# Kernel tuning notes

Hardware: AMD Instinct MI355X
Metric: run time of the kernel (lower is better)

Reference implementation:

```python
import jax, jax.numpy as jnp
import numpy as np

NEG_SLOPE = 0.2  # PyG GATConv default negative_slope
N_NODES = 40000
N_EDGES = 640000
IN_DIM = 128
SAT_DIM = 64
HID = 128
OUT_DIM = 54


def gat_conv(x, edge_index, W, a_src, a_dst, bias):
    """PyG GATConv with heads=1, concat=True, add_self_loops=True."""
    n = x.shape[0]
    loops = jnp.arange(n, dtype=edge_index.dtype)
    src = jnp.concatenate([edge_index[0], loops])  # message sources j
    dst = jnp.concatenate([edge_index[1], loops])  # message targets i
    h = x @ W.T                                    # [N, C]
    alpha_s = h @ a_src                            # [N]
    alpha_d = h @ a_dst                            # [N]
    e = jax.nn.leaky_relu(alpha_s[src] + alpha_d[dst], NEG_SLOPE)  # [E]
    # segment softmax over incoming edges of each dst node (self-loops guarantee non-empty segments)
    m = jax.ops.segment_max(e, dst, num_segments=n)
    e = jnp.exp(e - m[dst])
    denom = jax.ops.segment_sum(e, dst, num_segments=n)
    alpha = e / (denom[dst] + 1e-16)
    out = jax.ops.segment_sum(alpha[:, None] * h[src], dst, num_segments=n)
    return out + bias


def setup_inputs() -> dict:
    key = jax.random.key(0)
    ks = jax.random.split(key, 16)
    s = lambda d: 1.0 / np.sqrt(d)
    inp = {
        "x": jax.random.normal(ks[0], (N_NODES, IN_DIM), jnp.float32),
        "edge_index": jax.random.randint(ks[1], (2, N_EDGES), 0, N_NODES, jnp.int32),
        "sat_W": jax.random.normal(ks[2], (HID, SAT_DIM), jnp.float32) * s(SAT_DIM),
        "sat_b": jnp.zeros((HID,), jnp.float32),
        "neigh_W": jax.random.normal(ks[3], (HID, IN_DIM - SAT_DIM), jnp.float32) * s(IN_DIM - SAT_DIM),
        "neigh_b": jnp.zeros((HID,), jnp.float32),
        "conv1_W": jax.random.normal(ks[4], (HID, HID), jnp.float32) * s(HID),
        "conv1_asrc": jax.random.normal(ks[5], (HID,), jnp.float32) * s(HID),
        "conv1_adst": jax.random.normal(ks[6], (HID,), jnp.float32) * s(HID),
        "conv1_b": jnp.zeros((HID,), jnp.float32),
        "conv2_W": jax.random.normal(ks[7], (HID, HID), jnp.float32) * s(HID),
        "conv2_asrc": jax.random.normal(ks[8], (HID,), jnp.float32) * s(HID),
        "conv2_adst": jax.random.normal(ks[9], (HID,), jnp.float32) * s(HID),
        "conv2_b": jnp.zeros((HID,), jnp.float32),
        "fc1_W": jax.random.normal(ks[10], (HID, HID), jnp.float32) * s(HID),
        "fc1_b": jnp.zeros((HID,), jnp.float32),
        "fc2_W": jax.random.normal(ks[11], (OUT_DIM, HID), jnp.float32) * s(HID),
        "fc2_b": jnp.zeros((OUT_DIM,), jnp.float32),
    }
    return inp


def reference(x, edge_index, sat_W, sat_b, neigh_W, neigh_b,
              conv1_W, conv1_asrc, conv1_adst, conv1_b,
              conv2_W, conv2_asrc, conv2_adst, conv2_b,
              fc1_W, fc1_b, fc2_W, fc2_b):
    sat = jax.nn.relu(x[:, :SAT_DIM] @ sat_W.T + sat_b)
    nei = jax.nn.relu(x[:, SAT_DIM:] @ neigh_W.T + neigh_b)
    h = sat + 0.5 * nei
    h = jax.nn.relu(gat_conv(h, edge_index, conv1_W, conv1_asrc, conv1_adst, conv1_b))
    h = jax.nn.relu(gat_conv(h, edge_index, conv2_W, conv2_asrc, conv2_adst, conv2_b))
    h = jax.nn.relu(h @ fc1_W.T + fc1_b)
    return h @ fc2_W.T + fc2_b
```

## Files before the change

kernel.cpp:

```cpp
#include <hip/hip_runtime.h>


#define N_NODES 40000
#define N_EDGES 640000
#define DIM     128

typedef unsigned short u16;
typedef __attribute__((ext_vector_type(8))) short bf16x8;
typedef __attribute__((ext_vector_type(4))) float f32x4;

__device__ __forceinline__ u16 f2bf(float v) {
    unsigned u = __float_as_uint(v);
    u += 0x7FFFu + ((u >> 16) & 1u);
    return (u16)(u >> 16);
}
__device__ __forceinline__ float bf2f(u16 h) { return __uint_as_float(((unsigned)h) << 16); }
__device__ __forceinline__ float rdlane_f(float v, int l) {
    return __uint_as_float(__builtin_amdgcn_readlane(__float_as_uint(v), l));
}

__device__ __forceinline__ int hswz(int row, int col) {
    return row * 128 + ((((col >> 2) ^ (row & 7))) << 2) + (col & 3);
}
__device__ __forceinline__ float4 hread4(const float* hbuf, int row, int k) {
    int b = (k >> 2) ^ (row & 7);
    return *(const float4*)&hbuf[row * 128 + (b << 2)];
}
__device__ __forceinline__ void split8(const float* vv, bf16x8& hi, bf16x8& lo) {
#pragma unroll
    for (int i = 0; i < 8; ++i) {
        u16 h = f2bf(vv[i]);
        hi[i] = (short)h;
        lo[i] = (short)f2bf(vv[i] - bf2f(h));
    }
}

__global__ __launch_bounds__(256) void k_wcvt(
    const float* __restrict__ satW, const float* __restrict__ neiW,
    const float* __restrict__ c1W, const float* __restrict__ c2W,
    const float* __restrict__ f1W, const float* __restrict__ f2W,
    u16* __restrict__ wa, int* __restrict__ deg, int* __restrict__ counter) {
    int gid = (blockIdx.y * gridDim.x + blockIdx.x) * 256 + threadIdx.x;
    if (gid < N_NODES) deg[gid] = 1;
    if (gid == 0) *counter = 0;

    int m = blockIdx.y;
    const float* src; int C, K, Cp; int offH, offL;
    switch (m) {
        case 0: src = satW; C = 128; K = 64;  Cp = 128; offH = 0;      offL = 8192;   break;
        case 1: src = neiW; C = 128; K = 64;  Cp = 128; offH = 16384;  offL = 24576;  break;
        case 2: src = c1W;  C = 128; K = 128; Cp = 128; offH = 32768;  offL = 49152;  break;
        case 3: src = c2W;  C = 128; K = 128; Cp = 128; offH = 65536;  offL = 81920;  break;
        case 4: src = f1W;  C = 128; K = 128; Cp = 128; offH = 98304;  offL = 114688; break;
        default:src = f2W;  C = 54;  K = 128; Cp = 64;  offH = 131072; offL = 139264; break;
    }
    int e = blockIdx.x * 256 + threadIdx.x;
    if (e >= Cp * K) return;
    int c = e / K, k = e - c * K;
    float v = (c < C) ? src[c * K + k] : 0.f;
    u16 h = f2bf(v);
    wa[offH + e] = h;
    wa[offL + e] = f2bf(v - bf2f(h));
}

__global__ void k_deg_count(const int* __restrict__ dst, int* __restrict__ deg) {
    int t = blockIdx.x * 256 + threadIdx.x;
    if (t < N_EDGES) atomicAdd(&deg[dst[t]], 1);
}
__global__ void k_assign(const int* __restrict__ deg, int* __restrict__ counter,
                         int* __restrict__ start, int* __restrict__ cursor,
                         int* __restrict__ csr_src) {
    int i = blockIdx.x * 256 + threadIdx.x;
    if (i >= N_NODES) return;
    int d = deg[i];
    int s = atomicAdd(counter, d);
    start[i] = s;
    csr_src[s] = i;
    cursor[i] = s + 1;
}
__global__ void k_fill_edges(const int* __restrict__ src, const int* __restrict__ dst,
                             int* __restrict__ cursor, int* __restrict__ csr_src) {
    int t = blockIdx.x * 256 + threadIdx.x;
    if (t < N_EDGES) {
        int p = atomicAdd(&cursor[dst[t]], 1);
        csr_src[p] = src[t];
    }
}

template<int CT>
__device__ __forceinline__ void stage_W(u16* Ws, const u16* __restrict__ Wh,
                                        const u16* __restrict__ Wl, int kc, int tid) {
    for (int idx = tid; idx < CT * 2 * 2 * 64; idx += 256) {
        int l = idx & 63;
        int q = idx >> 6;
        int hilo = q & 1;
        int ks = (q >> 1) & 1;
        int ct = q >> 2;
        int c = ct * 16 + (l & 15);
        int k = kc * 64 + ks * 32 + (l >> 4) * 8;
        const u16* Wp = hilo ? Wl : Wh;
        *reinterpret_cast<bf16x8*>(&Ws[idx * 8]) =
            *reinterpret_cast<const bf16x8*>(Wp + (size_t)c * 128 + k);
    }
}

#define MFMA3(ACC, AH, AL, BH, BL)                                             \
    ACC = __builtin_amdgcn_mfma_f32_16x16x32_bf16(AH, BH, ACC, 0, 0, 0);       \
    ACC = __builtin_amdgcn_mfma_f32_16x16x32_bf16(AH, BL, ACC, 0, 0, 0);       \
    ACC = __builtin_amdgcn_mfma_f32_16x16x32_bf16(AL, BH, ACC, 0, 0, 0);

__device__ __forceinline__ void alpha_epi(const f32x4* acc, int lane, int r0,
                                          const float* __restrict__ a_src,
                                          const float* __restrict__ a_dst,
                                          float* __restrict__ as_, float* __restrict__ ad_) {
    float ps[4] = {0, 0, 0, 0}, pd[4] = {0, 0, 0, 0};
#pragma unroll
    for (int ct = 0; ct < 8; ++ct) {
        float asv = a_src[ct * 16 + (lane & 15)];
        float adv = a_dst[ct * 16 + (lane & 15)];
#pragma unroll
        for (int r = 0; r < 4; ++r) {
            ps[r] = fmaf(acc[ct][r], asv, ps[r]);
            pd[r] = fmaf(acc[ct][r], adv, pd[r]);
        }
    }
#pragma unroll
    for (int off = 1; off < 16; off <<= 1) {
#pragma unroll
        for (int r = 0; r < 4; ++r) {
            ps[r] += __shfl_xor(ps[r], off);
            pd[r] += __shfl_xor(pd[r], off);
        }
    }
    if ((lane & 15) == 0) {
#pragma unroll
        for (int r = 0; r < 4; ++r) {
            int row = r0 + (lane >> 4) * 4 + r;
            as_[row] = ps[r];
            ad_[row] = pd[r];
        }
    }
}

__global__ __launch_bounds__(256) void k_enc_conv1(
    const float* __restrict__ x,
    const u16* __restrict__ sH, const u16* __restrict__ sL,
    const u16* __restrict__ nH, const u16* __restrict__ nL,
    const float* __restrict__ satb, const float* __restrict__ neib,
    const u16* __restrict__ Wh, const u16* __restrict__ Wl,
    const float* __restrict__ a_src, const float* __restrict__ a_dst,
    u16* __restrict__ outG, float* __restrict__ as_, float* __restrict__ ad_)
{
    __shared__ u16 Wbuf[16384];
    __shared__ float hbuf[8192];
    const int tid = threadIdx.x, lane = tid & 63, wv = tid >> 6;
    const int r0 = blockIdx.x * 64 + wv * 16;
    const int arow = r0 + (lane & 15);
    const int kb = (lane >> 4) * 8;

    bf16x8 axh[4], axl[4];
#pragma unroll
    for (int s = 0; s < 4; ++s) {
        const float* p = x + (size_t)arow * 128 + s * 32 + kb;
        float4 a = *(const float4*)p;
        float4 b = *(const float4*)(p + 4);
        float vv[8] = {a.x, a.y, a.z, a.w, b.x, b.y, b.z, b.w};
        split8(vv, axh[s], axl[s]);
    }

    f32x4 accS[8], accN[8];
#pragma unroll
    for (int ct = 0; ct < 8; ++ct) { accS[ct] = (f32x4){0,0,0,0}; accN[ct] = (f32x4){0,0,0,0}; }

#pragma unroll
    for (int mat = 0; mat < 2; ++mat) {
        if (mat) __syncthreads();
        const u16* WH = mat ? nH : sH;
        const u16* WL = mat ? nL : sL;
        for (int idx = tid; idx < 2048; idx += 256) {
            int l = idx & 63;
            int q = idx >> 6;
            int hilo = q & 1;
            int ks = (q >> 1) & 1;
            int ct = q >> 2;
            int c = ct * 16 + (l & 15);
            int k = ks * 32 + (l >> 4) * 8;
            const u16* Wp = hilo ? WL : WH;
            *reinterpret_cast<bf16x8*>(&Wbuf[idx * 8]) =
                *reinterpret_cast<const bf16x8*>(Wp + (size_t)c * 64 + k);
        }
        __syncthreads();
#pragma unroll
        for (int ct = 0; ct < 8; ++ct) {
#pragma unroll
            for (int ks = 0; ks < 2; ++ks) {
                int s = mat * 2 + ks;
                int base = (ct * 2 + ks) * 1024;
                bf16x8 bh = *reinterpret_cast<const bf16x8*>(&Wbuf[base + lane * 8]);
                bf16x8 bl = *reinterpret_cast<const bf16x8*>(&Wbuf[base + 512 + lane * 8]);
                f32x4* ac = mat ? &accN[ct] : &accS[ct];
                MFMA3((*ac), axh[s], axl[s], bh, bl);
            }
        }
    }

#pragma unroll
    for (int ct = 0; ct < 8; ++ct) {
        int c = ct * 16 + (lane & 15);
        float bs = satb[c], bn = neib[c];
#pragma unroll
        for (int r = 0; r < 4; ++r) {
            int rl = wv * 16 + (lane >> 4) * 4 + r;
            float v = fmaxf(accS[ct][r] + bs, 0.f) + 0.5f * fmaxf(accN[ct][r] + bn, 0.f);
            hbuf[hswz(rl, c)] = v;
        }
    }
    __syncthreads();

    bf16x8 ah[4], al[4];
    const int ar = wv * 16 + (lane & 15);
#pragma unroll
    for (int s = 0; s < 4; ++s) {
        int k0 = s * 32 + kb;
        float4 a = hread4(hbuf, ar, k0);
        float4 b = hread4(hbuf, ar, k0 + 4);
        float vv[8] = {a.x, a.y, a.z, a.w, b.x, b.y, b.z, b.w};
        split8(vv, ah[s], al[s]);
    }

    f32x4 acc[8];
#pragma unroll
    for (int ct = 0; ct < 8; ++ct) acc[ct] = (f32x4){0, 0, 0, 0};
#pragma unroll
    for (int kc = 0; kc < 2; ++kc) {
        if (kc) __syncthreads();
        stage_W<8>(Wbuf, Wh, Wl, kc, tid);
        __syncthreads();
#pragma unroll
        for (int ct = 0; ct < 8; ++ct) {
#pragma unroll
            for (int ks = 0; ks < 2; ++ks) {
                int s = kc * 2 + ks;
                int base = (ct * 2 + ks) * 1024;
                bf16x8 bh = *reinterpret_cast<const bf16x8*>(&Wbuf[base + lane * 8]);
                bf16x8 bl = *reinterpret_cast<const bf16x8*>(&Wbuf[base + 512 + lane * 8]);
                MFMA3(acc[ct], ah[s], al[s], bh, bl);
            }
        }
    }

    alpha_epi(acc, lane, r0, a_src, a_dst, as_, ad_);

#pragma unroll
    for (int ct = 0; ct < 8; ++ct) {
        int c = ct * 16 + (lane & 15);
#pragma unroll
        for (int r = 0; r < 4; ++r) {
            int row = r0 + (lane >> 4) * 4 + r;
            outG[(size_t)row * 128 + c] = f2bf(acc[ct][r]);
        }
    }
}

__global__ __launch_bounds__(256) void k_conv_gemm(
    const u16* __restrict__ Ah, const u16* __restrict__ Al,
    const u16* __restrict__ Wh, const u16* __restrict__ Wl,
    const float* __restrict__ a_src, const float* __restrict__ a_dst,
    u16* __restrict__ outG, float* __restrict__ as_, float* __restrict__ ad_)
{
    __shared__ u16 Wbuf[16384];
    const int tid = threadIdx.x, lane = tid & 63, wv = tid >> 6;
    const int r0 = blockIdx.x * 64 + wv * 16;
    const int arow = r0 + (lane & 15);
    const int kb = (lane >> 4) * 8;

    bf16x8 ah[4], al[4];
#pragma unroll
    for (int s = 0; s < 4; ++s) {
        ah[s] = *reinterpret_cast<const bf16x8*>(Ah + (size_t)arow * 128 + s * 32 + kb);
        al[s] = *reinterpret_cast<const bf16x8*>(Al + (size_t)arow * 128 + s * 32 + kb);
    }

    f32x4 acc[8];
#pragma unroll
    for (int ct = 0; ct < 8; ++ct) acc[ct] = (f32x4){0, 0, 0, 0};
#pragma unroll
    for (int kc = 0; kc < 2; ++kc) {
        if (kc) __syncthreads();
        stage_W<8>(Wbuf, Wh, Wl, kc, tid);
        __syncthreads();
#pragma unroll
        for (int ct = 0; ct < 8; ++ct) {
#pragma unroll
            for (int ks = 0; ks < 2; ++ks) {
                int s = kc * 2 + ks;
                int base = (ct * 2 + ks) * 1024;
                bf16x8 bh = *reinterpret_cast<const bf16x8*>(&Wbuf[base + lane * 8]);
                bf16x8 bl = *reinterpret_cast<const bf16x8*>(&Wbuf[base + 512 + lane * 8]);
                MFMA3(acc[ct], ah[s], al[s], bh, bl);
            }
        }
    }

    alpha_epi(acc, lane, r0, a_src, a_dst, as_, ad_);

#pragma unroll
    for (int ct = 0; ct < 8; ++ct) {
        int c = ct * 16 + (lane & 15);
#pragma unroll
        for (int r = 0; r < 4; ++r) {
            int row = r0 + (lane >> 4) * 4 + r;
            outG[(size_t)row * 128 + c] = f2bf(acc[ct][r]);
        }
    }
}

__global__ __launch_bounds__(256) void k_fc12(
    const u16* __restrict__ Ah, const u16* __restrict__ Al,
    const u16* __restrict__ W1h, const u16* __restrict__ W1l, const float* __restrict__ b1,
    const u16* __restrict__ W2h, const u16* __restrict__ W2l, const float* __restrict__ b2,
    float* __restrict__ out)
{
    __shared__ u16 Wbuf[16384];
    __shared__ u16 W2buf[8192];
    float* hbuf = (float*)Wbuf;
    const int tid = threadIdx.x, lane = tid & 63, wv = tid >> 6;
    const int r0 = blockIdx.x * 64 + wv * 16;
    const int arow = r0 + (lane & 15);
    const int kb = (lane >> 4) * 8;

    bf16x8 ah[4], al[4];
#pragma unroll
    for (int s = 0; s < 4; ++s) {
        ah[s] = *reinterpret_cast<const bf16x8*>(Ah + (size_t)arow * 128 + s * 32 + kb);
        al[s] = *reinterpret_cast<const bf16x8*>(Al + (size_t)arow * 128 + s * 32 + kb);
    }

    f32x4 acc[8];
#pragma unroll
    for (int ct = 0; ct < 8; ++ct) acc[ct] = (f32x4){0, 0, 0, 0};
#pragma unroll
    for (int kc = 0; kc < 2; ++kc) {
        if (kc) __syncthreads();
        stage_W<8>(Wbuf, W1h, W1l, kc, tid);
        __syncthreads();
#pragma unroll
        for (int ct = 0; ct < 8; ++ct) {
#pragma unroll
            for (int ks = 0; ks < 2; ++ks) {
                int s = kc * 2 + ks;
                int base = (ct * 2 + ks) * 1024;
                bf16x8 bh = *reinterpret_cast<const bf16x8*>(&Wbuf[base + lane * 8]);
                bf16x8 bl = *reinterpret_cast<const bf16x8*>(&Wbuf[base + 512 + lane * 8]);
                MFMA3(acc[ct], ah[s], al[s], bh, bl);
            }
        }
    }
    __syncthreads();

#pragma unroll
    for (int ct = 0; ct < 8; ++ct) {
        int c = ct * 16 + (lane & 15);
        float bv = b1[c];
#pragma unroll
        for (int r = 0; r < 4; ++r) {
            int rl = wv * 16 + (lane >> 4) * 4 + r;
            hbuf[hswz(rl, c)] = fmaxf(acc[ct][r] + bv, 0.f);
        }
    }
    __syncthreads();

    bf16x8 a2h[4], a2l[4];
    const int ar = wv * 16 + (lane & 15);
#pragma unroll
    for (int s = 0; s < 4; ++s) {
        int k0 = s * 32 + kb;
        float4 a = hread4(hbuf, ar, k0);
        float4 b = hread4(hbuf, ar, k0 + 4);
        float vv[8] = {a.x, a.y, a.z, a.w, b.x, b.y, b.z, b.w};
        split8(vv, a2h[s], a2l[s]);
    }

    f32x4 acc2[4];
#pragma unroll
    for (int ct = 0; ct < 4; ++ct) acc2[ct] = (f32x4){0, 0, 0, 0};
#pragma unroll
    for (int kc = 0; kc < 2; ++kc) {
        if (kc) __syncthreads();
        stage_W<4>(W2buf, W2h, W2l, kc, tid);
        __syncthreads();
#pragma unroll
        for (int ct = 0; ct < 4; ++ct) {
#pragma unroll
            for (int ks = 0; ks < 2; ++ks) {
                int s = kc * 2 + ks;
                int base = (ct * 2 + ks) * 1024;
                bf16x8 bh = *reinterpret_cast<const bf16x8*>(&W2buf[base + lane * 8]);
                bf16x8 bl = *reinterpret_cast<const bf16x8*>(&W2buf[base + 512 + lane * 8]);
                MFMA3(acc2[ct], a2h[s], a2l[s], bh, bl);
            }
        }
    }

#pragma unroll
    for (int ct = 0; ct < 4; ++ct) {
        int c = ct * 16 + (lane & 15);
#pragma unroll
        for (int r = 0; r < 4; ++r) {
            int row = r0 + (lane >> 4) * 4 + r;
            if (c < 54) out[(size_t)row * 54 + c] = acc2[ct][r] + b2[c];
        }
    }
}

#define DO_PAIRS(NP, TB)                                                      \
    {                                                                         \
        float pw[NP]; const ushort4* hp[NP];                                  \
        _Pragma("unroll")                                                     \
        for (int q = 0; q < NP; ++q) {                                        \
            int e0 = (TB) + 2 * q;                                            \
            float plo = rdlane_f(p, e0), phi = rdlane_f(p, e0 + 1);           \
            int jlo = __builtin_amdgcn_readlane(jj, e0);                      \
            int jhi = __builtin_amdgcn_readlane(jj, e0 + 1);                  \
            pw[q] = hodd ? phi : plo;                                         \
            int j = hodd ? jhi : jlo;                                         \
            hp[q] = (const ushort4*)&hg[(size_t)j * 128 + 4 * l32];           \
        }                                                                     \
        ushort4 hv[NP];                                                       \
        _Pragma("unroll") for (int q = 0; q < NP; ++q) hv[q] = *hp[q];        \
        _Pragma("unroll") for (int q = 0; q < NP; ++q) {                      \
            acc.x = fmaf(pw[q], bf2f(hv[q].x), acc.x);                        \
            acc.y = fmaf(pw[q], bf2f(hv[q].y), acc.y);                        \
            acc.z = fmaf(pw[q], bf2f(hv[q].z), acc.z);                        \
            acc.w = fmaf(pw[q], bf2f(hv[q].w), acc.w);                        \
        }                                                                     \
    }

__global__ __launch_bounds__(256) void k_aggregate(
    const u16* __restrict__ hg, const float* __restrict__ as_,
    const float* __restrict__ ad_, const int* __restrict__ start,
    const int* __restrict__ deg, const int* __restrict__ csr_src,
    const float* __restrict__ bias, u16* __restrict__ outH, u16* __restrict__ outL)
{
    int wid = (blockIdx.x * 256 + threadIdx.x) >> 6;
    int lane = threadIdx.x & 63;
    if (wid >= N_NODES) return;

    const int s0 = start[wid];
    const int s1 = s0 + deg[wid];
    const float adi = ad_[wid];
    const int l32 = lane & 31;
    const bool hodd = lane >= 32;

    float4 acc = make_float4(0.f, 0.f, 0.f, 0.f);
    float ssum = 0.f;
    for (int base = s0; base < s1; base += 64) {
        int k = base + lane;
        int cnt = min(64, s1 - base);
        int jj = 0;
        float p = 0.f;
        if (k < s1) {
            jj = csr_src[k];
            float e = as_[jj] + adi;
            e = (e > 0.f) ? e : 0.2f * e;
            p = __expf(e);
            ssum += p;
        }
        int t = 0;
        for (; t + 16 <= cnt; t += 16) DO_PAIRS(8, t)
        if (t + 8 <= cnt) { DO_PAIRS(4, t) t += 8; }
        if (t + 4 <= cnt) { DO_PAIRS(2, t) t += 4; }
        for (; t < cnt; t += 2) DO_PAIRS(1, t)
    }
#pragma unroll
    for (int off = 32; off; off >>= 1) ssum += __shfl_xor(ssum, off);
    acc.x += __shfl_xor(acc.x, 32);
    acc.y += __shfl_xor(acc.y, 32);
    acc.z += __shfl_xor(acc.z, 32);
    acc.w += __shfl_xor(acc.w, 32);
    float inv = 1.f / (ssum + 1e-16f);

    if (!hodd) {
        float4 bv = *(const float4*)&bias[4 * l32];
        float o0 = fmaxf(fmaf(acc.x, inv, bv.x), 0.f);
        float o1 = fmaxf(fmaf(acc.y, inv, bv.y), 0.f);
        float o2 = fmaxf(fmaf(acc.z, inv, bv.z), 0.f);
        float o3 = fmaxf(fmaf(acc.w, inv, bv.w), 0.f);
        u16 h0 = f2bf(o0), h1 = f2bf(o1), h2 = f2bf(o2), h3 = f2bf(o3);
        ushort4 hvv = make_ushort4(h0, h1, h2, h3);
        ushort4 lvv = make_ushort4(f2bf(o0 - bf2f(h0)), f2bf(o1 - bf2f(h1)),
                                   f2bf(o2 - bf2f(h2)), f2bf(o3 - bf2f(h3)));
        *(ushort4*)&outH[(size_t)wid * 128 + 4 * l32] = hvv;
        *(ushort4*)&outL[(size_t)wid * 128 + 4 * l32] = lvv;
    }
}

extern "C" void kernel_launch(void* const* d_in, const int* in_sizes, int n_in,
                              void* d_out, int out_size, void* d_ws, size_t ws_size,
                              hipStream_t stream) {
    (void)in_sizes; (void)n_in; (void)out_size; (void)ws_size;

    const float* x       = (const float*)d_in[0];
    const int*   ei      = (const int*)d_in[1];
    const float* sat_W   = (const float*)d_in[2];
    const float* sat_b   = (const float*)d_in[3];
    const float* neigh_W = (const float*)d_in[4];
    const float* neigh_b = (const float*)d_in[5];
    const float* c1_W    = (const float*)d_in[6];
    const float* c1_as   = (const float*)d_in[7];
    const float* c1_ad   = (const float*)d_in[8];
    const float* c1_b    = (const float*)d_in[9];
    const float* c2_W    = (const float*)d_in[10];
    const float* c2_as   = (const float*)d_in[11];
    const float* c2_ad   = (const float*)d_in[12];
    const float* c2_b    = (const float*)d_in[13];
    const float* fc1_W   = (const float*)d_in[14];
    const float* fc1_b   = (const float*)d_in[15];
    const float* fc2_W   = (const float*)d_in[16];
    const float* fc2_b   = (const float*)d_in[17];

    const int* e_src = ei;
    const int* e_dst = ei + N_EDGES;

    char* w = (char*)d_ws;
    u16*   hG     = (u16*)  (w);
    u16*   hH     = (u16*)  (w + 10240000);
    u16*   hL     = (u16*)  (w + 20480000);
    float* as_    = (float*)(w + 30720000);
    float* ad_    = (float*)(w + 30880000);
    int*   deg    = (int*)  (w + 31040000);
    int*   start  = (int*)  (w + 31200000);
    int*   cursor = (int*)  (w + 31360000);
    int*   counter= (int*)  (w + 31520000);
    int*   csr    = (int*)  (w + 31520256);
    u16*   wa     = (u16*)  (w + 34240256);

    u16 *satH = wa,          *satL = wa + 8192;
    u16 *neiH = wa + 16384,  *neiL = wa + 24576;
    u16 *c1H  = wa + 32768,  *c1L  = wa + 49152;
    u16 *c2H  = wa + 65536,  *c2L  = wa + 81920;
    u16 *f1H  = wa + 98304,  *f1L  = wa + 114688;
    u16 *f2H  = wa + 131072, *f2L  = wa + 139264;

    dim3 b(256);
    k_wcvt<<<dim3(64, 6), b, 0, stream>>>(sat_W, neigh_W, c1_W, c2_W, fc1_W, fc2_W,
                                          wa, deg, counter);
    k_deg_count <<<2500, b, 0, stream>>>(e_dst, deg);
    k_assign    <<<157,  b, 0, stream>>>(deg, counter, start, cursor, csr);
    k_fill_edges<<<2500, b, 0, stream>>>(e_src, e_dst, cursor, csr);

    k_enc_conv1<<<625, b, 0, stream>>>(x, satH, satL, neiH, neiL, sat_b, neigh_b,
                                       c1H, c1L, c1_as, c1_ad, hG, as_, ad_);
    k_aggregate<<<10000, b, 0, stream>>>(hG, as_, ad_, start, deg, csr, c1_b, hH, hL);

    k_conv_gemm<<<625, b, 0, stream>>>(hH, hL, c2H, c2L, c2_as, c2_ad, hG, as_, ad_);
    k_aggregate<<<10000, b, 0, stream>>>(hG, as_, ad_, start, deg, csr, c2_b, hH, hL);

    k_fc12<<<625, b, 0, stream>>>(hH, hL, f1H, f1L, fc1_b, f2H, f2L, fc2_b,
                                  (float*)d_out);
}
```

Before: 213.3 us.

## Split GEMM tiles by column across waves and read weights directly from global

The dense GEMM kernels (encoder+conv1, conv2, fc1+fc2) now use 32-row blocks in which each of the four waves handles 16 rows by 64 columns, and the grid size doubles. Weight fragments are loaded straight from global memory (served by L2) into registers instead of being staged through shared memory with barriers. The attention-coefficient row sums are combined across the two column groups through a small shared reduction buffer. The goal is lower LDS use, fewer syncs, fewer accumulators per wave and better occupancy, at the cost of more global weight traffic per block and A-fragment reloads duplicated across column groups.

```diff
diff --git a/kernel.cpp b/kernel.cpp
--- a/kernel.cpp
+++ b/kernel.cpp
@@ -34,6 +34,14 @@
         lo[i] = (short)f2bf(vv[i] - bf2f(h));
     }
 }
+__device__ __forceinline__ bf16x8 ldb(const u16* p) {
+    return *reinterpret_cast<const bf16x8*>(p);
+}
+
+#define MFMA3(ACC, AH, AL, BH, BL)                                             \
+    ACC = __builtin_amdgcn_mfma_f32_16x16x32_bf16(AH, BH, ACC, 0, 0, 0);       \
+    ACC = __builtin_amdgcn_mfma_f32_16x16x32_bf16(AH, BL, ACC, 0, 0, 0);       \
+    ACC = __builtin_amdgcn_mfma_f32_16x16x32_bf16(AL, BH, ACC, 0, 0, 0);
 
 __global__ __launch_bounds__(256) void k_wcvt(
     const float* __restrict__ satW, const float* __restrict__ neiW,
@@ -87,37 +95,15 @@
     }
 }
 
-template<int CT>
-__device__ __forceinline__ void stage_W(u16* Ws, const u16* __restrict__ Wh,
-                                        const u16* __restrict__ Wl, int kc, int tid) {
-    for (int idx = tid; idx < CT * 2 * 2 * 64; idx += 256) {
-        int l = idx & 63;
-        int q = idx >> 6;
-        int hilo = q & 1;
-        int ks = (q >> 1) & 1;
-        int ct = q >> 2;
-        int c = ct * 16 + (l & 15);
-        int k = kc * 64 + ks * 32 + (l >> 4) * 8;
-        const u16* Wp = hilo ? Wl : Wh;
-        *reinterpret_cast<bf16x8*>(&Ws[idx * 8]) =
-            *reinterpret_cast<const bf16x8*>(Wp + (size_t)c * 128 + k);
-    }
-}
-
-#define MFMA3(ACC, AH, AL, BH, BL)                                             \
-    ACC = __builtin_amdgcn_mfma_f32_16x16x32_bf16(AH, BH, ACC, 0, 0, 0);       \
-    ACC = __builtin_amdgcn_mfma_f32_16x16x32_bf16(AH, BL, ACC, 0, 0, 0);       \
-    ACC = __builtin_amdgcn_mfma_f32_16x16x32_bf16(AL, BH, ACC, 0, 0, 0);
-
-__device__ __forceinline__ void alpha_epi(const f32x4* acc, int lane, int r0,
-                                          const float* __restrict__ a_src,
-                                          const float* __restrict__ a_dst,
-                                          float* __restrict__ as_, float* __restrict__ ad_) {
+__device__ __forceinline__ void alpha_colsplit(
+    const f32x4* acc, int lane, int colgrp, int rowgrp, int tid, int brow0,
+    const float* __restrict__ a_src, const float* __restrict__ a_dst,
+    float (*redbuf)[2][32], float* __restrict__ as_, float* __restrict__ ad_) {
     float ps[4] = {0, 0, 0, 0}, pd[4] = {0, 0, 0, 0};
 #pragma unroll
-    for (int ct = 0; ct < 8; ++ct) {
-        float asv = a_src[ct * 16 + (lane & 15)];
-        float adv = a_dst[ct * 16 + (lane & 15)];
+    for (int ct = 0; ct < 4; ++ct) {
+        int c = colgrp * 64 + ct * 16 + (lane & 15);
+        float asv = a_src[c], adv = a_dst[c];
 #pragma unroll
         for (int r = 0; r < 4; ++r) {
             ps[r] = fmaf(acc[ct][r], asv, ps[r]);
@@ -135,10 +121,15 @@
     if ((lane & 15) == 0) {
 #pragma unroll
         for (int r = 0; r < 4; ++r) {
-            int row = r0 + (lane >> 4) * 4 + r;
-            as_[row] = ps[r];
-            ad_[row] = pd[r];
-        }
+            int rl = rowgrp * 16 + (lane >> 4) * 4 + r;
+            redbuf[0][colgrp][rl] = ps[r];
+            redbuf[1][colgrp][rl] = pd[r];
+        }
+    }
+    __syncthreads();
+    if (tid < 32) {
+        as_[brow0 + tid] = redbuf[0][0][tid] + redbuf[0][1][tid];
+        ad_[brow0 + tid] = redbuf[1][0][tid] + redbuf[1][1][tid];
     }
 }
 
@@ -151,12 +142,15 @@
     const float* __restrict__ a_src, const float* __restrict__ a_dst,
     u16* __restrict__ outG, float* __restrict__ as_, float* __restrict__ ad_)
 {
-    __shared__ u16 Wbuf[16384];
-    __shared__ float hbuf[8192];
+    __shared__ float hbuf[32 * 128];
+    __shared__ float redbuf[2][2][32];
     const int tid = threadIdx.x, lane = tid & 63, wv = tid >> 6;
-    const int r0 = blockIdx.x * 64 + wv * 16;
+    const int rowgrp = wv >> 1, colgrp = wv & 1;
+    const int brow0 = blockIdx.x * 32;
+    const int r0 = brow0 + rowgrp * 16;
     const int arow = r0 + (lane & 15);
     const int kb = (lane >> 4) * 8;
+    const int cb = colgrp * 64 + (lane & 15);
 
     bf16x8 axh[4], axl[4];
 #pragma unroll
@@ -168,49 +162,27 @@
         split8(vv, axh[s], axl[s]);
     }
 
-    f32x4 accS[8], accN[8];
-#pragma unroll
-    for (int ct = 0; ct < 8; ++ct) { accS[ct] = (f32x4){0,0,0,0}; accN[ct] = (f32x4){0,0,0,0}; }
-
-#pragma unroll
-    for (int mat = 0; mat < 2; ++mat) {
-        if (mat) __syncthreads();
-        const u16* WH = mat ? nH : sH;
-        const u16* WL = mat ? nL : sL;
-        for (int idx = tid; idx < 2048; idx += 256) {
-            int l = idx & 63;
-            int q = idx >> 6;
-            int hilo = q & 1;
-            int ks = (q >> 1) & 1;
-            int ct = q >> 2;
-            int c = ct * 16 + (l & 15);
-            int k = ks * 32 + (l >> 4) * 8;
-            const u16* Wp = hilo ? WL : WH;
-            *reinterpret_cast<bf16x8*>(&Wbuf[idx * 8]) =
-                *reinterpret_cast<const bf16x8*>(Wp + (size_t)c * 64 + k);
-        }
-        __syncthreads();
-#pragma unroll
-        for (int ct = 0; ct < 8; ++ct) {
-#pragma unroll
-            for (int ks = 0; ks < 2; ++ks) {
-                int s = mat * 2 + ks;
-                int base = (ct * 2 + ks) * 1024;
-                bf16x8 bh = *reinterpret_cast<const bf16x8*>(&Wbuf[base + lane * 8]);
-                bf16x8 bl = *reinterpret_cast<const bf16x8*>(&Wbuf[base + 512 + lane * 8]);
-                f32x4* ac = mat ? &accN[ct] : &accS[ct];
-                MFMA3((*ac), axh[s], axl[s], bh, bl);
-            }
-        }
-    }
-
-#pragma unroll
-    for (int ct = 0; ct < 8; ++ct) {
-        int c = ct * 16 + (lane & 15);
+    f32x4 accS[4], accN[4];
+#pragma unroll
+    for (int ct = 0; ct < 4; ++ct) { accS[ct] = (f32x4){0,0,0,0}; accN[ct] = (f32x4){0,0,0,0}; }
+#pragma unroll
+    for (int ct = 0; ct < 4; ++ct) {
+        int c = cb + ct * 16;
+#pragma unroll
+        for (int ks = 0; ks < 2; ++ks) {
+            size_t wo = (size_t)c * 64 + ks * 32 + kb;
+            MFMA3(accS[ct], axh[ks], axl[ks], ldb(sH + wo), ldb(sL + wo));
+            MFMA3(accN[ct], axh[ks + 2], axl[ks + 2], ldb(nH + wo), ldb(nL + wo));
+        }
+    }
+
+#pragma unroll
+    for (int ct = 0; ct < 4; ++ct) {
+        int c = cb + ct * 16;
         float bs = satb[c], bn = neib[c];
 #pragma unroll
         for (int r = 0; r < 4; ++r) {
-            int rl = wv * 16 + (lane >> 4) * 4 + r;
+            int rl = rowgrp * 16 + (lane >> 4) * 4 + r;
             float v = fmaxf(accS[ct][r] + bs, 0.f) + 0.5f * fmaxf(accN[ct][r] + bn, 0.f);
             hbuf[hswz(rl, c)] = v;
         }
@@ -218,7 +190,7 @@
     __syncthreads();
 
     bf16x8 ah[4], al[4];
-    const int ar = wv * 16 + (lane & 15);
+    const int ar = rowgrp * 16 + (lane & 15);
 #pragma unroll
     for (int s = 0; s < 4; ++s) {
         int k0 = s * 32 + kb;
@@ -228,32 +200,24 @@
         split8(vv, ah[s], al[s]);
     }
 
-    f32x4 acc[8];
-#pragma unroll
-    for (int ct = 0; ct < 8; ++ct) acc[ct] = (f32x4){0, 0, 0, 0};
-#pragma unroll
-    for (int kc = 0; kc < 2; ++kc) {
-        if (kc) __syncthreads();
-        stage_W<8>(Wbuf, Wh, Wl, kc, tid);
-        __syncthreads();
-#pragma unroll
-        for (int ct = 0; ct < 8; ++ct) {
-#pragma unroll
-            for (int ks = 0; ks < 2; ++ks) {
-                int s = kc * 2 + ks;
-                int base = (ct * 2 + ks) * 1024;
-                bf16x8 bh = *reinterpret_cast<const bf16x8*>(&Wbuf[base + lane * 8]);
-                bf16x8 bl = *reinterpret_cast<const bf16x8*>(&Wbuf[base + 512 + lane * 8]);
-                MFMA3(acc[ct], ah[s], al[s], bh, bl);
-            }
-        }
-    }
-
-    alpha_epi(acc, lane, r0, a_src, a_dst, as_, ad_);
-
-#pragma unroll
-    for (int ct = 0; ct < 8; ++ct) {
-        int c = ct * 16 + (lane & 15);
+    f32x4 acc[4];
+#pragma unroll
+    for (int ct = 0; ct < 4; ++ct) acc[ct] = (f32x4){0, 0, 0, 0};
+#pragma unroll
+    for (int ct = 0; ct < 4; ++ct) {
+        int c = cb + ct * 16;
+#pragma unroll
+        for (int s = 0; s < 4; ++s) {
+            size_t wo = (size_t)c * 128 + s * 32 + kb;
+            MFMA3(acc[ct], ah[s], al[s], ldb(Wh + wo), ldb(Wl + wo));
+        }
+    }
+
+    alpha_colsplit(acc, lane, colgrp, rowgrp, tid, brow0, a_src, a_dst, redbuf, as_, ad_);
+
+#pragma unroll
+    for (int ct = 0; ct < 4; ++ct) {
+        int c = cb + ct * 16;
 #pragma unroll
         for (int r = 0; r < 4; ++r) {
             int row = r0 + (lane >> 4) * 4 + r;
@@ -268,45 +232,40 @@
     const float* __restrict__ a_src, const float* __restrict__ a_dst,
     u16* __restrict__ outG, float* __restrict__ as_, float* __restrict__ ad_)
 {
-    __shared__ u16 Wbuf[16384];
+    __shared__ float redbuf[2][2][32];
     const int tid = threadIdx.x, lane = tid & 63, wv = tid >> 6;
-    const int r0 = blockIdx.x * 64 + wv * 16;
+    const int rowgrp = wv >> 1, colgrp = wv & 1;
+    const int brow0 = blockIdx.x * 32;
+    const int r0 = brow0 + rowgrp * 16;
     const int arow = r0 + (lane & 15);
     const int kb = (lane >> 4) * 8;
+    const int cb = colgrp * 64 + (lane & 15);
 
     bf16x8 ah[4], al[4];
 #pragma unroll
     for (int s = 0; s < 4; ++s) {
-        ah[s] = *reinterpret_cast<const bf16x8*>(Ah + (size_t)arow * 128 + s * 32 + kb);
-        al[s] = *reinterpret_cast<const bf16x8*>(Al + (size_t)arow * 128 + s * 32 + kb);
-    }
-
-    f32x4 acc[8];
-#pragma unroll
-    for (int ct = 0; ct < 8; ++ct) acc[ct] = (f32x4){0, 0, 0, 0};
-#pragma unroll
-    for (int kc = 0; kc < 2; ++kc) {
-        if (kc) __syncthreads();
-        stage_W<8>(Wbuf, Wh, Wl, kc, tid);
-        __syncthreads();
-#pragma unroll
-        for (int ct = 0; ct < 8; ++ct) {
-#pragma unroll
-            for (int ks = 0; ks < 2; ++ks) {
-                int s = kc * 2 + ks;
-                int base = (ct * 2 + ks) * 1024;
-                bf16x8 bh = *reinterpret_cast<const bf16x8*>(&Wbuf[base + lane * 8]);
-                bf16x8 bl = *reinterpret_cast<const bf16x8*>(&Wbuf[base + 512 + lane * 8]);
-                MFMA3(acc[ct], ah[s], al[s], bh, bl);
-            }
-        }
-    }
-
-    alpha_epi(acc, lane, r0, a_src, a_dst, as_, ad_);
-
-#pragma unroll
-    for (int ct = 0; ct < 8; ++ct) {
-        int c = ct * 16 + (lane & 15);
+        ah[s] = ldb(Ah + (size_t)arow * 128 + s * 32 + kb);
+        al[s] = ldb(Al + (size_t)arow * 128 + s * 32 + kb);
+    }
+
+    f32x4 acc[4];
+#pragma unroll
+    for (int ct = 0; ct < 4; ++ct) acc[ct] = (f32x4){0, 0, 0, 0};
+#pragma unroll
+    for (int ct = 0; ct < 4; ++ct) {
+        int c = cb + ct * 16;
+#pragma unroll
+        for (int s = 0; s < 4; ++s) {
+            size_t wo = (size_t)c * 128 + s * 32 + kb;
+            MFMA3(acc[ct], ah[s], al[s], ldb(Wh + wo), ldb(Wl + wo));
+        }
+    }
+
+    alpha_colsplit(acc, lane, colgrp, rowgrp, tid, brow0, a_src, a_dst, redbuf, as_, ad_);
+
+#pragma unroll
+    for (int ct = 0; ct < 4; ++ct) {
+        int c = cb + ct * 16;
 #pragma unroll
         for (int r = 0; r < 4; ++r) {
             int row = r0 + (lane >> 4) * 4 + r;
@@ -321,57 +280,48 @@
     const u16* __restrict__ W2h, const u16* __restrict__ W2l, const float* __restrict__ b2,
     float* __restrict__ out)
 {
-    __shared__ u16 Wbuf[16384];
-    __shared__ u16 W2buf[8192];
-    float* hbuf = (float*)Wbuf;
+    __shared__ float hbuf[32 * 128];
     const int tid = threadIdx.x, lane = tid & 63, wv = tid >> 6;
-    const int r0 = blockIdx.x * 64 + wv * 16;
+    const int rowgrp = wv >> 1, colgrp = wv & 1;
+    const int r0 = blockIdx.x * 32 + rowgrp * 16;
     const int arow = r0 + (lane & 15);
     const int kb = (lane >> 4) * 8;
+    const int cb = colgrp * 64 + (lane & 15);
 
     bf16x8 ah[4], al[4];
 #pragma unroll
     for (int s = 0; s < 4; ++s) {
-        ah[s] = *reinterpret_cast<const bf16x8*>(Ah + (size_t)arow * 128 + s * 32 + kb);
-        al[s] = *reinterpret_cast<const bf16x8*>(Al + (size_t)arow * 128 + s * 32 + kb);
-    }
-
-    f32x4 acc[8];
-#pragma unroll
-    for (int ct = 0; ct < 8; ++ct) acc[ct] = (f32x4){0, 0, 0, 0};
-#pragma unroll
-    for (int kc = 0; kc < 2; ++kc) {
-        if (kc) __syncthreads();
-        stage_W<8>(Wbuf, W1h, W1l, kc, tid);
-        __syncthreads();
-#pragma unroll
-        for (int ct = 0; ct < 8; ++ct) {
-#pragma unroll
-            for (int ks = 0; ks < 2; ++ks) {
-                int s = kc * 2 + ks;
-                int base = (ct * 2 + ks) * 1024;
-                bf16x8 bh = *reinterpret_cast<const bf16x8*>(&Wbuf[base + lane * 8]);
-                bf16x8 bl = *reinterpret_cast<const bf16x8*>(&Wbuf[base + 512 + lane * 8]);
-                MFMA3(acc[ct], ah[s], al[s], bh, bl);
-            }
+        ah[s] = ldb(Ah + (size_t)arow * 128 + s * 32 + kb);
+        al[s] = ldb(Al + (size_t)arow * 128 + s * 32 + kb);
+    }
+
+    f32x4 acc[4];
+#pragma unroll
+    for (int ct = 0; ct < 4; ++ct) acc[ct] = (f32x4){0, 0, 0, 0};
+#pragma unroll
+    for (int ct = 0; ct < 4; ++ct) {
+        int c = cb + ct * 16;
+#pragma unroll
+        for (int s = 0; s < 4; ++s) {
+            size_t wo = (size_t)c * 128 + s * 32 + kb;
+            MFMA3(acc[ct], ah[s], al[s], ldb(W1h + wo), ldb(W1l + wo));
+        }
+    }
+
+#pragma unroll
+    for (int ct = 0; ct < 4; ++ct) {
+        int c = cb + ct * 16;
+        float bv = b1[c];
+#pragma unroll
+        for (int r = 0; r < 4; ++r) {
+            int rl = rowgrp * 16 + (lane >> 4) * 4 + r;
+            hbuf[hswz(rl, c)] = fmaxf(acc[ct][r] + bv, 0.f);
         }
     }
     __syncthreads();
 
-#pragma unroll
-    for (int ct = 0; ct < 8; ++ct) {
-        int c = ct * 16 + (lane & 15);
-        float bv = b1[c];
-#pragma unroll
-        for (int r = 0; r < 4; ++r) {
-            int rl = wv * 16 + (lane >> 4) * 4 + r;
-            hbuf[hswz(rl, c)] = fmaxf(acc[ct][r] + bv, 0.f);
-        }
-    }
-    __syncthreads();
-
     bf16x8 a2h[4], a2l[4];
-    const int ar = wv * 16 + (lane & 15);
+    const int ar = rowgrp * 16 + (lane & 15);
 #pragma unroll
     for (int s = 0; s < 4; ++s) {
         int k0 = s * 32 + kb;
@@ -381,30 +331,22 @@
         split8(vv, a2h[s], a2l[s]);
     }
 
-    f32x4 acc2[4];
-#pragma unroll
-    for (int ct = 0; ct < 4; ++ct) acc2[ct] = (f32x4){0, 0, 0, 0};
-#pragma unroll
-    for (int kc = 0; kc < 2; ++kc) {
-        if (kc) __syncthreads();
-        stage_W<4>(W2buf, W2h, W2l, kc, tid);
-        __syncthreads();
-#pragma unroll
-        for (int ct = 0; ct < 4; ++ct) {
-#pragma unroll
-            for (int ks = 0; ks < 2; ++ks) {
-                int s = kc * 2 + ks;
-                int base = (ct * 2 + ks) * 1024;
-                bf16x8 bh = *reinterpret_cast<const bf16x8*>(&W2buf[base + lane * 8]);
-                bf16x8 bl = *reinterpret_cast<const bf16x8*>(&W2buf[base + 512 + lane * 8]);
-                MFMA3(acc2[ct], a2h[s], a2l[s], bh, bl);
-            }
-        }
-    }
-
-#pragma unroll
-    for (int ct = 0; ct < 4; ++ct) {
-        int c = ct * 16 + (lane & 15);
+    f32x4 acc2[2];
+#pragma unroll
+    for (int ct = 0; ct < 2; ++ct) acc2[ct] = (f32x4){0, 0, 0, 0};
+#pragma unroll
+    for (int ct = 0; ct < 2; ++ct) {
+        int c = colgrp * 32 + ct * 16 + (lane & 15);
+#pragma unroll
+        for (int s = 0; s < 4; ++s) {
+            size_t wo = (size_t)c * 128 + s * 32 + kb;
+            MFMA3(acc2[ct], a2h[s], a2l[s], ldb(W2h + wo), ldb(W2l + wo));
+        }
+    }
+
+#pragma unroll
+    for (int ct = 0; ct < 2; ++ct) {
+        int c = colgrp * 32 + ct * 16 + (lane & 15);
 #pragma unroll
         for (int r = 0; r < 4; ++r) {
             int row = r0 + (lane >> 4) * 4 + r;
@@ -549,13 +491,13 @@
     k_assign    <<<157,  b, 0, stream>>>(deg, counter, start, cursor, csr);
     k_fill_edges<<<2500, b, 0, stream>>>(e_src, e_dst, cursor, csr);
 
-    k_enc_conv1<<<625, b, 0, stream>>>(x, satH, satL, neiH, neiL, sat_b, neigh_b,
-                                       c1H, c1L, c1_as, c1_ad, hG, as_, ad_);
+    k_enc_conv1<<<1250, b, 0, stream>>>(x, satH, satL, neiH, neiL, sat_b, neigh_b,
+                                        c1H, c1L, c1_as, c1_ad, hG, as_, ad_);
     k_aggregate<<<10000, b, 0, stream>>>(hG, as_, ad_, start, deg, csr, c1_b, hH, hL);
 
-    k_conv_gemm<<<625, b, 0, stream>>>(hH, hL, c2H, c2L, c2_as, c2_ad, hG, as_, ad_);
+    k_conv_gemm<<<1250, b, 0, stream>>>(hH, hL, c2H, c2L, c2_as, c2_ad, hG, as_, ad_);
     k_aggregate<<<10000, b, 0, stream>>>(hG, as_, ad_, start, deg, csr, c2_b, hH, hL);
 
-    k_fc12<<<625, b, 0, stream>>>(hH, hL, f1H, f1L, fc1_b, f2H, f2L, fc2_b,
-                                  (float*)d_out);
-}
+    k_fc12<<<1250, b, 0, stream>>>(hH, hL, f1H, f1L, fc1_b, f2H, f2L, fc2_b,
+                                   (float*)d_out);
+}
```

Result: slower. 250.5 us (+17.4%).
